# Kernel optimization log

Hardware: AMD Instinct MI355X
Metric: run time of the kernel (lower is better)

## Reference

```python
import jax, jax.numpy as jnp
import numpy as np

GAMMA = 0.5      # temperature from __init__
SOS_ID = 2       # constant <sos> token id
EPS = 1e-10


def setup_inputs() -> dict:
    key = jax.random.key(0)
    ks = jax.random.split(key, 12)
    B, T, E, DY, DZ, V = 64, 32, 100, 200, 500, 32000
    H = DY + DZ
    s = lambda k, shape, sc=1.0: (jax.random.normal(k, shape, jnp.float32) * sc)
    return {
        "z": s(ks[0], (B, DZ), 0.1),
        "labels": jax.random.uniform(ks[1], (B,), jnp.float32),
        "W_fc": s(ks[2], (DY, 1), 0.1),
        "b_fc": s(ks[3], (DY,), 0.1),
        "embed_weight": s(ks[4], (V, E), 0.1),
        "W_ih": s(ks[5], (3 * H, E), 0.05),
        "W_hh": s(ks[6], (3 * H, H), 0.05),
        "b_ih": s(ks[7], (3 * H,), 0.05),
        "b_hh": s(ks[8], (3 * H,), 0.05),
        "W_out": s(ks[9], (V, H), 0.05),
        "b_out": s(ks[10], (V,), 0.05),
        "gumbel_u": jax.random.uniform(ks[11], (T - 1, B, V), jnp.float32),
        "src": jax.random.randint(jax.random.fold_in(key, 99), (T, B), 0, V),
        "src_len": T,
    }


def _gru_step(h, x, W_ih, W_hh, b_ih, b_hh):
    # PyTorch GRU cell: gates ordered (r, z, n)
    gi = x @ W_ih.T + b_ih          # [B, 3H]
    gh = h @ W_hh.T + b_hh          # [B, 3H]
    i_r, i_z, i_n = jnp.split(gi, 3, axis=-1)
    h_r, h_z, h_n = jnp.split(gh, 3, axis=-1)
    r = jax.nn.sigmoid(i_r + h_r)
    zt = jax.nn.sigmoid(i_z + h_z)
    n = jnp.tanh(i_n + r * h_n)
    return (1.0 - zt) * n + zt * h


def reference(z, labels, W_fc, b_fc, embed_weight, W_ih, W_hh, b_ih, b_hh,
              W_out, b_out, gumbel_u, src, src_len):
    B, H = z.shape[0], W_hh.shape[1]
    V = W_out.shape[0]
    # h0 = cat(fc(1 - labels), z)
    h0 = jnp.concatenate([(1.0 - labels)[:, None] @ W_fc.T + b_fc, z], axis=-1)  # [B, H]
    x0 = jnp.broadcast_to(embed_weight[SOS_ID], (B, embed_weight.shape[1]))      # [B, E]

    def step(carry, u):
        h, x = carry
        h = _gru_step(h, x, W_ih, W_hh, b_ih, b_hh)      # [B, H]
        pred = h @ W_out.T + b_out                        # [B, V]
        g = -jnp.log(-jnp.log(u + EPS) + EPS)             # gumbel noise
        y = jax.nn.softmax(pred + g, axis=-1)             # gumbel_softmax, tau=1
        x_next = (y / GAMMA) @ embed_weight               # soft embedding [B, E]
        return (h, x_next), (h, pred)

    (_, _), (outs, preds) = jax.lax.scan(step, (h0, x0), gumbel_u)  # [T-1,B,H], [T-1,B,V]

    dt = z.dtype
    outputs = jnp.concatenate(
        [h0[None], jnp.zeros((1, B, H), dt), outs], axis=0)         # [T+1, B, H]
    predictions = jnp.concatenate(
        [jnp.zeros((1, B, V), dt), preds], axis=0)                  # [T, B, V]
    return outputs, predictions
```

## Files before the change

kernel.cpp:

```cpp
#include <hip/hip_runtime.h>

#define B 64
#define TS 31
#define E 100
#define DY 200
#define DZ 500
#define V 32000
#define H 700
#define HP 704
#define H3 2100
#define XH 800
#define SOS 2
#define OUT_PRED_OFF (33*B*H)
#define NPB 500
#define VCH 125
#define NVCH 256
#define SOFF 15.0f

typedef unsigned short u16;
typedef __attribute__((ext_vector_type(8))) short short8;
typedef __attribute__((ext_vector_type(4))) float f32x4;

__device__ __forceinline__ float sigm(float x) { return 1.f / (1.f + __expf(-x)); }
__device__ __forceinline__ u16 f2b(float f) {
  union { float f; unsigned int u; } c; c.f = f;
  unsigned int u = c.u;
  u16 h = (u16)(u >> 16);
  unsigned int rem = u & 0xFFFFu;
  h += (u16)((rem > 0x8000u) || (rem == 0x8000u && (h & 1)));
  return h;
}

__global__ __launch_bounds__(256) void k_zero(float* __restrict__ out, long n) {
  long i0 = (long)blockIdx.x * 256 + threadIdx.x;
  long st = (long)gridDim.x * 256;
  for (long i = i0; i < n; i += st) out[i] = 0.f;
}

__global__ __launch_bounds__(256) void k0_init(
    const float* __restrict__ z, const float* __restrict__ labels,
    const float* __restrict__ W_fc, const float* __restrict__ b_fc,
    const float* __restrict__ embed, const float* __restrict__ W_ih,
    const float* __restrict__ W_hh, const float* __restrict__ W_out,
    float* __restrict__ out, float* __restrict__ hA, float* __restrict__ WT,
    u16* __restrict__ W2, u16* __restrict__ h_bf,
    float* __restrict__ xacc, float* __restrict__ Zp, float* __restrict__ gh)
{
  long i0 = (long)blockIdx.x * 256 + threadIdx.x;
  long st = (long)gridDim.x * 256;
  for (long i = i0; i < (long)NPB * B; i += st) Zp[i] = 2.f / (float)NPB;
  for (long i = i0; i < (long)B * H3; i += st) gh[i] = 0.f;
  for (long i = i0; i < (long)B * V; i += st) out[OUT_PRED_OFF + i] = 0.f;
  for (long i = i0; i < (long)B * H; i += st) out[B * H + i] = 0.f;
  for (long i = i0; i < (long)B * H; i += st) {
    int b = (int)(i / H), j = (int)(i % H);
    float v = (j < DY) ? (1.f - labels[b]) * W_fc[j] + b_fc[j]
                       : z[b * DZ + (j - DY)];
    hA[i] = v;
    out[i] = v;
  }
  for (long i = i0; i < (long)B * E; i += st) {
    int e = (int)(i % E);
    xacc[i] = embed[SOS * E + e];
  }
  for (long i = i0; i < (long)B * HP; i += st) h_bf[i] = 0;
  for (long i = i0; i < (long)XH * H3; i += st) {
    int k = (int)(i / H3), g = (int)(i % H3);
    WT[i] = (k < E) ? W_ih[(long)g * E + k] : W_hh[(long)g * H + (k - E)];
  }
  for (long i = i0; i < (long)V * HP; i += st) {
    long s8 = i >> 3; int j = (int)(i & 7);
    int lane = (int)(s8 & 63);
    long tmp = s8 >> 6;
    int kk = (int)(tmp % 22);
    long cgrp = tmp / 22;
    int col = (int)(cgrp * 16 + (lane & 15));
    int k = kk * 32 + ((lane >> 4) << 3) + j;
    W2[i] = (k < H) ? f2b(W_out[(size_t)col * H + k]) : (u16)0;
  }
}

__global__ __launch_bounds__(256) void k1a(
    const float* __restrict__ xacc, const float* __restrict__ Zp,
    const float* __restrict__ hin, const float* __restrict__ WT,
    const float* __restrict__ b_ih,
    float* __restrict__ gig, float* __restrict__ gh)
{
  int nt = blockIdx.x, c = blockIdx.y;
  int n = nt * 32 + (threadIdx.x & 31);
  int bq = threadIdx.x >> 5;
  __shared__ float xs[64][100];
  __shared__ float invZ[64];
  if (c == 0) {
    if (threadIdx.x < 64) {
      float s = 0.f;
      for (int u = 0; u < NPB; ++u) s += Zp[(size_t)u * 64 + threadIdx.x];
      invZ[threadIdx.x] = 2.f / s;
    }
    __syncthreads();
  }
  for (int i = threadIdx.x; i < 6400; i += 256) {
    int b = i / 100, kk = i % 100;
    xs[b][kk] = (c == 0) ? xacc[i] * invZ[b] : hin[b * H + (c - 1) * 100 + kk];
  }
  __syncthreads();
  if (n >= H3) return;
  float acc[8];
  #pragma unroll
  for (int bb = 0; bb < 8; ++bb) acc[bb] = 0.f;
  for (int kk = 0; kk < 100; ++kk) {
    float w = WT[(size_t)(c * 100 + kk) * H3 + n];
    #pragma unroll
    for (int bb = 0; bb < 8; ++bb) acc[bb] += xs[bq * 8 + bb][kk] * w;
  }
  if (c == 0) {
    float bi = b_ih[n];
    #pragma unroll
    for (int bb = 0; bb < 8; ++bb) gig[(size_t)(bq * 8 + bb) * H3 + n] = acc[bb] + bi;
  } else {
    #pragma unroll
    for (int bb = 0; bb < 8; ++bb)
      atomicAdd(&gh[(size_t)(bq * 8 + bb) * H3 + n], acc[bb]);
  }
}

__global__ __launch_bounds__(256) void k1br(
    const float* __restrict__ gig, float* __restrict__ gh,
    const float* __restrict__ b_hh, const float* __restrict__ hin,
    float* __restrict__ hout, float* __restrict__ out_h, u16* __restrict__ h_bf,
    float* __restrict__ xacc)
{
  int i = blockIdx.x * 256 + threadIdx.x;
  if (i >= B * H) return;
  if (i < B * E) xacc[i] = 0.f;
  int b = i / H, j = i % H;
  size_t g0 = (size_t)b * H3 + j;
  float ir = gig[g0], iz = gig[g0 + H], in_ = gig[g0 + 2 * H];
  float hr = gh[g0] + b_hh[j];
  float hz = gh[g0 + H] + b_hh[H + j];
  float hn = gh[g0 + 2 * H] + b_hh[2 * H + j];
  gh[g0] = 0.f; gh[g0 + H] = 0.f; gh[g0 + 2 * H] = 0.f;
  float hprev = hin[b * H + j];
  float r  = sigm(ir + hr);
  float zt = sigm(iz + hz);
  float nn = tanhf(in_ + r * hn);
  float hv = (1.f - zt) * nn + zt * hprev;
  hout[b * H + j] = hv;
  out_h[i] = hv;
  h_bf[b * HP + j] = f2b(hv);
}

__global__ __launch_bounds__(256) void k2(
    const u16* __restrict__ h_bf, const u16* __restrict__ W2,
    const float* __restrict__ b_out, const float* __restrict__ gu,
    float* __restrict__ pred, float* __restrict__ w_f, float* __restrict__ Zp)
{
  __shared__ float lzp[64][4];
  const int u = blockIdx.x, tid = threadIdx.x;
  const int wave = tid >> 6, lane = tid & 63, l15 = lane & 15;
  const int col = u * 64 + wave * 16 + l15;
  f32x4 acc[4];
  #pragma unroll
  for (int q = 0; q < 4; ++q) acc[q] = f32x4{0.f, 0.f, 0.f, 0.f};
  const short8* wv2 = (const short8*)W2 + ((size_t)(u * 4 + wave) * 22) * 64 + lane;
  const u16* hp = h_bf + ((lane >> 4) << 3);
  for (int kk = 0; kk < 22; ++kk) {
    short8 bv = wv2[(size_t)kk * 64];
    #pragma unroll
    for (int rt = 0; rt < 4; ++rt) {
      short8 a = *reinterpret_cast<const short8*>(hp + (size_t)(rt * 16 + l15) * HP + kk * 32);
      acc[rt] = __builtin_amdgcn_mfma_f32_16x16x32_bf16(a, bv, acc[rt], 0, 0, 0);
    }
  }
  float bo = b_out[col];
  #pragma unroll
  for (int rt = 0; rt < 4; ++rt) {
    #pragma unroll
    for (int r = 0; r < 4; ++r) {
      int brow = rt * 16 + ((lane >> 4) << 2) + r;
      float pv = acc[rt][r] + bo;
      size_t off = (size_t)brow * V + col;
      __builtin_nontemporal_store(pv, &pred[off]);
      float uu = __builtin_nontemporal_load(&gu[off]);
      float g = -__logf(-__logf(uu + 1e-10f) + 1e-10f);
      float w = __expf(pv + g - SOFF);
      __builtin_nontemporal_store(w, &w_f[off]);
      float vz = w;
      vz += __shfl_xor(vz, 1); vz += __shfl_xor(vz, 2);
      vz += __shfl_xor(vz, 4); vz += __shfl_xor(vz, 8);
      if (l15 == 0) lzp[brow][wave] = vz;
    }
  }
  __syncthreads();
  if (tid < 64)
    Zp[(size_t)u * 64 + tid] = lzp[tid][0] + lzp[tid][1] + lzp[tid][2] + lzp[tid][3];
}

__global__ __launch_bounds__(256) void k3(
    const float* __restrict__ w_f, const float* __restrict__ embed,
    float* __restrict__ xacc)
{
  int c = blockIdx.x;
  int v0 = c * VCH;
  int e = threadIdx.x & 127, bh = threadIdx.x >> 7;
  __shared__ float ys[64][VCH];
  for (int i = threadIdx.x; i < 64 * VCH; i += 256) {
    int b = i / VCH, vv = i % VCH;
    ys[b][vv] = w_f[(size_t)b * V + v0 + vv];
  }
  __syncthreads();
  if (e >= E) return;
  float acc[32];
  #pragma unroll
  for (int bb = 0; bb < 32; ++bb) acc[bb] = 0.f;
  for (int vv = 0; vv < VCH; ++vv) {
    float w = embed[(size_t)(v0 + vv) * E + e];
    #pragma unroll
    for (int bb = 0; bb < 32; ++bb) acc[bb] += ys[bh * 32 + bb][vv] * w;
  }
  #pragma unroll
  for (int bb = 0; bb < 32; ++bb)
    atomicAdd(&xacc[(size_t)(bh * 32 + bb) * E + e], acc[bb]);
}

extern "C" void kernel_launch(void* const* d_in, const int* in_sizes, int n_in,
                              void* d_out, int out_size, void* d_ws, size_t ws_size,
                              hipStream_t stream) {
  (void)ws_size;
  float* out = (float*)d_out;

  static const long lsz[12] = {32000, 64, 200, 200, 3200000, 210000, 1470000,
                               2100, 2100, 22400000, 32000, 63488000};
  static const int dictP[12]    = {0, 1, 2, 3, 4, 5, 6, 7, 8, 9, 10, 11};
  static const int alpha14P[12] = {13, 10, 0, 4, 8, 2, 1, 6, 5, 3, 7, 9};
  static const int alpha12P[12] = {11, 10, 0, 4, 8, 2, 1, 6, 5, 3, 7, 9};
  auto okperm = [&](const int* p) -> bool {
    for (int i = 0; i < 12; ++i) {
      if (p[i] >= n_in) return false;
      if ((long)in_sizes[p[i]] != lsz[i]) return false;
    }
    return true;
  };
  const int* P_ = nullptr;
  if (okperm(dictP)) P_ = dictP;
  else if (okperm(alpha14P)) P_ = alpha14P;
  else if (okperm(alpha12P)) P_ = alpha12P;
  if (!P_) { k_zero<<<2048, 256, 0, stream>>>(out, (long)out_size); return; }

  const float* z      = (const float*)d_in[P_[0]];
  const float* labels = (const float*)d_in[P_[1]];
  const float* W_fc   = (const float*)d_in[P_[2]];
  const float* b_fc   = (const float*)d_in[P_[3]];
  const float* embed  = (const float*)d_in[P_[4]];
  const float* W_ih   = (const float*)d_in[P_[5]];
  const float* W_hh   = (const float*)d_in[P_[6]];
  const float* b_ih   = (const float*)d_in[P_[7]];
  const float* b_hh   = (const float*)d_in[P_[8]];
  const float* W_out  = (const float*)d_in[P_[9]];
  const float* b_out  = (const float*)d_in[P_[10]];
  const float* gu     = (const float*)d_in[P_[11]];

  char* w = (char*)d_ws;
  auto alloc = [&](size_t bytes) { char* p = w; w += (bytes + 255) & ~(size_t)255; return p; };
  float* hA    = (float*)alloc((size_t)B * H * 4);
  float* hB    = (float*)alloc((size_t)B * H * 4);
  float* WT    = (float*)alloc((size_t)XH * H3 * 4);
  float* gig   = (float*)alloc((size_t)B * H3 * 4);
  float* gh    = (float*)alloc((size_t)B * H3 * 4);
  float* w_f   = (float*)alloc((size_t)B * V * 4);
  float* Zp    = (float*)alloc((size_t)NPB * B * 4);
  float* xacc  = (float*)alloc((size_t)B * E * 4);
  u16*  W2     = (u16*)alloc((size_t)V * HP * 2);
  u16*  h_bf   = (u16*)alloc((size_t)B * HP * 2);

  k0_init<<<2048, 256, 0, stream>>>(z, labels, W_fc, b_fc, embed, W_ih, W_hh, W_out,
                                    out, hA, WT, W2, h_bf, xacc, Zp, gh);

  for (int t = 0; t < TS; ++t) {
    float* hin  = (t & 1) ? hB : hA;
    float* hout = (t & 1) ? hA : hB;
    float* pred = out + OUT_PRED_OFF + (size_t)(1 + t) * B * V;
    k1a<<<dim3(66, 8), 256, 0, stream>>>(xacc, Zp, hin, WT, b_ih, gig, gh);
    k1br<<<(B * H + 255) / 256, 256, 0, stream>>>(gig, gh, b_hh, hin, hout,
                                                  out + (size_t)(2 + t) * B * H, h_bf,
                                                  xacc);
    k2<<<NPB, 256, 0, stream>>>(h_bf, W2, b_out, gu + (size_t)t * B * V,
                                pred, w_f, Zp);
    if (t < TS - 1)
      k3<<<NVCH, 256, 0, stream>>>(w_f, embed, xacc);
  }
}
```

Before: 3.718 ms.

## Replace atomic soft-embedding accumulation with per-block partials and a reduction kernel

The soft-embedding GEMV kernel now runs 128 blocks that each cover 250 vocab rows and write per-block partial sums to a workspace buffer, instead of 256 blocks doing atomicAdd into xacc. A new small kernel sums the 128 partials into xacc, so the zeroing of xacc in the GRU kernel is no longer needed. The w_f store in the logits kernel also changes from nontemporal to a normal store, so k3 may find it in cache. This removes contention from float atomics at the cost of an extra launch per step, a larger workspace buffer and halved parallelism in k3.

```diff
diff --git a/kernel.cpp b/kernel.cpp
--- a/kernel.cpp
+++ b/kernel.cpp
@@ -13,8 +13,7 @@
 #define SOS 2
 #define OUT_PRED_OFF (33*B*H)
 #define NPB 500
-#define VCH 125
-#define NVCH 256
+#define NEB 128
 #define SOFF 15.0f
 
 typedef unsigned short u16;
@@ -127,12 +126,10 @@
 __global__ __launch_bounds__(256) void k1br(
     const float* __restrict__ gig, float* __restrict__ gh,
     const float* __restrict__ b_hh, const float* __restrict__ hin,
-    float* __restrict__ hout, float* __restrict__ out_h, u16* __restrict__ h_bf,
-    float* __restrict__ xacc)
+    float* __restrict__ hout, float* __restrict__ out_h, u16* __restrict__ h_bf)
 {
   int i = blockIdx.x * 256 + threadIdx.x;
   if (i >= B * H) return;
-  if (i < B * E) xacc[i] = 0.f;
   int b = i / H, j = i % H;
   size_t g0 = (size_t)b * H3 + j;
   float ir = gig[g0], iz = gig[g0 + H], in_ = gig[g0 + 2 * H];
@@ -184,7 +181,7 @@
       float uu = __builtin_nontemporal_load(&gu[off]);
       float g = -__logf(-__logf(uu + 1e-10f) + 1e-10f);
       float w = __expf(pv + g - SOFF);
-      __builtin_nontemporal_store(w, &w_f[off]);
+      w_f[off] = w;
       float vz = w;
       vz += __shfl_xor(vz, 1); vz += __shfl_xor(vz, 2);
       vz += __shfl_xor(vz, 4); vz += __shfl_xor(vz, 8);
@@ -198,29 +195,47 @@
 
 __global__ __launch_bounds__(256) void k3(
     const float* __restrict__ w_f, const float* __restrict__ embed,
-    float* __restrict__ xacc)
-{
-  int c = blockIdx.x;
-  int v0 = c * VCH;
-  int e = threadIdx.x & 127, bh = threadIdx.x >> 7;
-  __shared__ float ys[64][VCH];
-  for (int i = threadIdx.x; i < 64 * VCH; i += 256) {
-    int b = i / VCH, vv = i % VCH;
-    ys[b][vv] = w_f[(size_t)b * V + v0 + vv];
-  }
-  __syncthreads();
-  if (e >= E) return;
+    float* __restrict__ P)
+{
+  const int u = blockIdx.x;
+  const int e = threadIdx.x & 127, bh = threadIdx.x >> 7;
+  __shared__ float ys[64][125];
   float acc[32];
   #pragma unroll
   for (int bb = 0; bb < 32; ++bb) acc[bb] = 0.f;
-  for (int vv = 0; vv < VCH; ++vv) {
-    float w = embed[(size_t)(v0 + vv) * E + e];
-    #pragma unroll
-    for (int bb = 0; bb < 32; ++bb) acc[bb] += ys[bh * 32 + bb][vv] * w;
-  }
-  #pragma unroll
-  for (int bb = 0; bb < 32; ++bb)
-    atomicAdd(&xacc[(size_t)(bh * 32 + bb) * E + e], acc[bb]);
+  for (int p = 0; p < 2; ++p) {
+    if (p) __syncthreads();
+    int v0 = u * 250 + p * 125;
+    for (int i = threadIdx.x; i < 64 * 125; i += 256) {
+      int b = i / 125, vv = i % 125;
+      ys[b][vv] = w_f[(size_t)b * V + v0 + vv];
+    }
+    __syncthreads();
+    if (e < E) {
+      for (int vv = 0; vv < 125; ++vv) {
+        float w = embed[(size_t)(v0 + vv) * E + e];
+        #pragma unroll
+        for (int bb = 0; bb < 32; ++bb) acc[bb] += ys[bh * 32 + bb][vv] * w;
+      }
+    }
+  }
+  if (e < E) {
+    float* pu = P + (size_t)u * (B * E);
+    #pragma unroll
+    for (int bb = 0; bb < 32; ++bb)
+      pu[(size_t)(bh * 32 + bb) * E + e] = acc[bb];
+  }
+}
+
+__global__ __launch_bounds__(256) void k4(
+    const float* __restrict__ P, float* __restrict__ xacc)
+{
+  int i = blockIdx.x * 256 + threadIdx.x;
+  if (i >= B * E) return;
+  float s = 0.f;
+  #pragma unroll 4
+  for (int u = 0; u < NEB; ++u) s += P[(size_t)u * (B * E) + i];
+  xacc[i] = s;
 }
 
 extern "C" void kernel_launch(void* const* d_in, const int* in_sizes, int n_in,
@@ -270,6 +285,7 @@
   float* w_f   = (float*)alloc((size_t)B * V * 4);
   float* Zp    = (float*)alloc((size_t)NPB * B * 4);
   float* xacc  = (float*)alloc((size_t)B * E * 4);
+  float* Pp    = (float*)alloc((size_t)NEB * B * E * 4);
   u16*  W2     = (u16*)alloc((size_t)V * HP * 2);
   u16*  h_bf   = (u16*)alloc((size_t)B * HP * 2);
 
@@ -282,11 +298,12 @@
     float* pred = out + OUT_PRED_OFF + (size_t)(1 + t) * B * V;
     k1a<<<dim3(66, 8), 256, 0, stream>>>(xacc, Zp, hin, WT, b_ih, gig, gh);
     k1br<<<(B * H + 255) / 256, 256, 0, stream>>>(gig, gh, b_hh, hin, hout,
-                                                  out + (size_t)(2 + t) * B * H, h_bf,
-                                                  xacc);
+                                                  out + (size_t)(2 + t) * B * H, h_bf);
     k2<<<NPB, 256, 0, stream>>>(h_bf, W2, b_out, gu + (size_t)t * B * V,
                                 pred, w_f, Zp);
-    if (t < TS - 1)
-      k3<<<NVCH, 256, 0, stream>>>(w_f, embed, xacc);
-  }
-}
+    if (t < TS - 1) {
+      k3<<<NEB, 256, 0, stream>>>(w_f, embed, Pp);
+      k4<<<25, 256, 0, stream>>>(Pp, xacc);
+    }
+  }
+}
```

Result: slower. 5.101 ms (+37.2%).
